# Kernel optimization log

Measured on AMD Instinct MI355X. Metric: run time of the kernel, lower is better.

The kernel has to match this reference:

```python
import jax, jax.numpy as jnp
import numpy as np

LRELU_SLOPE = 0.2
ACT_GAIN = float(np.sqrt(2.0))  # def_gain of lrelu in StyleGAN2
CLAMP = 256.0


def _affine(w, W, b):
    # StyleGAN2 FullyConnectedLayer: runtime weight gain 1/sqrt(in_features)
    return w @ W.T * (1.0 / np.sqrt(W.shape[1])) + b[None, :]


def _gather(x, fn, pad):
    # zero rows for padding faces appended at the end, then neighborhood gather
    padded = jnp.concatenate([x, jnp.zeros((pad, x.shape[1]), x.dtype)], axis=0)
    return padded[fn]  # [N, K, C]


def _mod_texture_conv(g, styles, wc, wsd, wcr):
    # g: [N, 9, I] gathered neighborhoods; styles: [B, I]
    B, I = styles.shape
    N = g.shape[0]
    F = N // B
    # position-typed 1x1 weights: [self, 4 sides, 4 corners] -> [O, I, 9]
    W = jnp.concatenate([wc[:, :, None],
                         jnp.repeat(wsd[:, :, None], 4, axis=2),
                         jnp.repeat(wcr[:, :, None], 4, axis=2)], axis=2)
    wmod = W[None] * styles[:, None, :, None]                    # [B,O,I,9] modulate
    d = jax.lax.rsqrt(jnp.sum(wmod * wmod, axis=(2, 3)) + 1e-8)  # [B,O] demodulate
    wmod = wmod * d[:, :, None, None]
    out = jnp.einsum('bfki,boik->bfok', g.reshape(B, F, 9, I), wmod)
    return out.max(axis=3).reshape(N, -1)  # MaxPool2d((1,9)) aggregation


def _smooth_upsample(x, pool_map, fn, pad):
    # replicate coarse face features to fine faces, then smooth over 9-neighborhood
    return _gather(x[pool_map], fn, pad).mean(axis=1)


def _act(x, bias):
    # clamp_gain(lrelu(x+b), act_gain*gain, 256*gain) with gain=1
    return jnp.clip(jax.nn.leaky_relu(x + bias[None, :], LRELU_SLOPE) * ACT_GAIN, -CLAMP, CLAMP)


def setup_inputs() -> dict:
    key = jax.random.key(0)
    ks = iter(jax.random.split(key, 40))
    B, Fc, Ff = 1, 32768, 131072
    IN, OUT, GEO, COL, WD = 128, 128, 32, 3, 512
    OC1 = OUT - GEO  # 96
    PAD0, PAD1 = 1024, 4096
    nk = lambda *s: jax.random.normal(next(ks), s, jnp.float32)
    ri = lambda shape, hi: jax.random.randint(next(ks), shape, 0, hi, jnp.int32).astype(jnp.int64)
    return dict(
        x=nk(B * Fc, IN - GEO), shape_feat=nk(B * Fc, GEO), img=nk(B * Fc, COL),
        ws=nk(B, 3, WD),
        fn0=ri((B * Fc, 9), B * Fc + PAD0), fn1=ri((B * Ff, 9), B * Ff + PAD1),
        pool_map0=ri((B * Ff,), B * Fc),
        pad0=PAD0, pad1=PAD1,
        affine0_w=nk(IN, WD), affine0_b=jnp.ones((IN,), jnp.float32),
        w_center0=nk(OUT, IN), w_side0=nk(OUT, IN), w_corner0=nk(OUT, IN),
        noise_strength0=nk(1) * 0.1, bias0=nk(OUT) * 0.1, noise_const0=nk(Ff),
        affine1_w=nk(OUT, WD), affine1_b=jnp.ones((OUT,), jnp.float32),
        w_center1=nk(OC1, OUT), w_side1=nk(OC1, OUT), w_corner1=nk(OC1, OUT),
        noise_strength1=nk(1) * 0.1, bias1=nk(OC1) * 0.1, noise_const1=nk(Ff),
        affine2_w=nk(OC1, WD), affine2_b=jnp.ones((OC1,), jnp.float32),
        w_rgb=nk(COL, OC1), bias_rgb=nk(COL) * 0.1,
    )


def reference(x, shape_feat, img, ws, fn0, fn1, pool_map0, pad0, pad1,
              affine0_w, affine0_b, w_center0, w_side0, w_corner0,
              noise_strength0, bias0, noise_const0,
              affine1_w, affine1_b, w_center1, w_side1, w_corner1,
              noise_strength1, bias1, noise_const1,
              affine2_w, affine2_b, w_rgb, bias_rgb):
    B = ws.shape[0]
    h = jnp.concatenate([x, shape_feat], axis=1)  # [B*Fc, IN]
    # ---- conv0: coarse-level modulated face conv, then SmoothUpsample to fine ----
    s0 = _affine(ws[:, 0], affine0_w, affine0_b)
    h = _mod_texture_conv(_gather(h, fn0, pad0), s0, w_center0, w_side0, w_corner0)
    h = _smooth_upsample(h, pool_map0, fn1, pad1)  # [B*Ff, OUT]
    h = h + jnp.tile(noise_const0[None, :], (B, 1)).reshape(-1, 1) * noise_strength0
    h = _act(h, bias0)
    # ---- conv1: fine-level modulated face conv ----
    s1 = _affine(ws[:, 1], affine1_w, affine1_b)
    h = _mod_texture_conv(_gather(h, fn1, pad1), s1, w_center1, w_side1, w_corner1)
    h = h + jnp.tile(noise_const1[None, :], (B, 1)).reshape(-1, 1) * noise_strength1
    h = _act(h, bias1)  # [B*Ff, 96]
    # ---- torgb: 1x1 modulated conv (demodulate=False), weight_gain on styles ----
    s2 = _affine(ws[:, 2], affine2_w, affine2_b) * (1.0 / np.sqrt(w_rgb.shape[1]))
    xg = _gather(h, fn1[:, :1], pad1)[:, 0]  # kernel_size^2 == 1 -> self gather
    y = jnp.einsum('bfi,oi,bi->bfo', xg.reshape(B, -1, xg.shape[1]), w_rgb, s2)
    y = jnp.clip(y.reshape(xg.shape[0], -1) + bias_rgb[None, :], -CLAMP, CLAMP)
    img_out = _smooth_upsample(img, pool_map0, fn1, pad1) + y
    return h, img_out
```

## Files before the change

kernel.cpp:

```cpp
#include <hip/hip_runtime.h>

#define FC 32768
#define FF 131072
#define LRELU_SLOPE 0.2f
#define ACT_GAIN 1.4142135623730951f
#define CLAMP_V 256.0f

typedef __bf16 bf16x8 __attribute__((ext_vector_type(8)));
typedef float f32x4 __attribute__((ext_vector_type(4)));
typedef float f32x2 __attribute__((ext_vector_type(2)));
typedef unsigned u32x4 __attribute__((ext_vector_type(4)));
typedef unsigned u32x2 __attribute__((ext_vector_type(2)));
typedef unsigned short u16x4 __attribute__((ext_vector_type(4)));

static __device__ __forceinline__ unsigned short f2bf(float f) {
    unsigned u = __float_as_uint(f);
    u += 0x7FFFu + ((u >> 16) & 1u);
    return (unsigned short)(u >> 16);
}
static __device__ __forceinline__ unsigned packbf(float a, float b) {
    return (unsigned)f2bf(a) | ((unsigned)f2bf(b) << 16);
}
static __device__ __forceinline__ float bf2f(unsigned short u) {
    return __uint_as_float(((unsigned)u) << 16);
}
static __device__ __forceinline__ float actf(float v) {
    v = (v < 0.f) ? v * LRELU_SLOPE : v;
    v *= ACT_GAIN;
    return fminf(fmaxf(v, -CLAMP_V), CLAMP_V);
}

__global__ void k_prep2(const float* __restrict__ wsvec,
                        const float* __restrict__ a0w, const float* __restrict__ a0b,
                        const float* __restrict__ a1w, const float* __restrict__ a1b,
                        const float* __restrict__ a2w, const float* __restrict__ a2b,
                        float* __restrict__ s0, float* __restrict__ s1, float* __restrict__ s2,
                        unsigned* __restrict__ zrow)
{
    int lane = threadIdx.x & 63;
    int t = blockIdx.x * 4 + (threadIdx.x >> 6);
    if (t >= 352) {
        if (t == 352) zrow[lane] = 0u;
        return;
    }
    int level, o;
    const float *W, *bptr; float* out;
    if (t < 128)       { level = 0; o = t;       W = a0w; bptr = a0b; out = s0; }
    else if (t < 256)  { level = 1; o = t - 128; W = a1w; bptr = a1b; out = s1; }
    else               { level = 2; o = t - 256; W = a2w; bptr = a2b; out = s2; }
    const float* wrow = wsvec + level * 512;
    const float* Wr = W + (size_t)o * 512;
    f32x4 wa = *(const f32x4*)(wrow + lane * 8);
    f32x4 wb = *(const f32x4*)(wrow + lane * 8 + 4);
    f32x4 va = *(const f32x4*)(Wr + lane * 8);
    f32x4 vb = *(const f32x4*)(Wr + lane * 8 + 4);
    float acc = wa.x * va.x + wa.y * va.y + wa.z * va.z + wa.w * va.w
              + wb.x * vb.x + wb.y * vb.y + wb.z * vb.z + wb.w * vb.w;
    #pragma unroll
    for (int off = 32; off; off >>= 1) acc += __shfl_down(acc, off, 64);
    if (lane == 0) {
        float v = acc * 0.04419417382415922f + bptr[o];
        if (level == 2) v *= 0.10206207261596577f;
        out[o] = v;
    }
}

__global__ void k_misc(const float* __restrict__ x, const float* __restrict__ sf,
                       u16x4* __restrict__ xcat,
                       const int* __restrict__ fn1, const int* __restrict__ pmap,
                       int* __restrict__ cidx)
{
    int b = blockIdx.x;
    if (b < FC * 32 / 256) {
        int gid = b * 256 + threadIdx.x;
        int f = gid >> 5;
        int c4 = (gid & 31) * 4;
        f32x4 v;
        if (c4 < 96) v = *(const f32x4*)(x + (size_t)f * 96 + c4);
        else         v = *(const f32x4*)(sf + (size_t)f * 32 + (c4 - 96));
        u16x4 o;
        o.x = f2bf(v.x); o.y = f2bf(v.y); o.z = f2bf(v.z); o.w = f2bf(v.w);
        xcat[gid] = o;
    } else {
        int gid = (b - FC * 32 / 256) * 256 + threadIdx.x;
        int g = fn1[gid];
        cidx[gid] = ((unsigned)g < FF) ? pmap[g] : -1;
    }
}

__global__ void k_wmod(const float* __restrict__ wc0, const float* __restrict__ wsd0,
                       const float* __restrict__ wcr0, const float* __restrict__ s0,
                       unsigned short* __restrict__ wm0,
                       const float* __restrict__ wc1, const float* __restrict__ wsd1,
                       const float* __restrict__ wcr1, const float* __restrict__ s1,
                       unsigned short* __restrict__ wm1,
                       const float* __restrict__ wrgb, const float* __restrict__ s2,
                       float* __restrict__ wrgbmod)
{
    int b = blockIdx.x;
    int i = threadIdx.x;
    if (b == 224) {
        for (int t = i; t < 288; t += 128) {
            int c = t / 96, k = t % 96;
            wrgbmod[c * 96 + k] = wrgb[c * 96 + k] * s2[k];
        }
        return;
    }
    const float *wc, *wsd, *wcr, *s; unsigned short* out; int o, O;
    if (b < 128) { wc = wc0; wsd = wsd0; wcr = wcr0; s = s0; out = wm0; o = b; O = 128; }
    else         { wc = wc1; wsd = wsd1; wcr = wcr1; s = s1; out = wm1; o = b - 128; O = 96; }
    float sv = s[i];
    float pc = wc[o * 128 + i] * sv;
    float ps = wsd[o * 128 + i] * sv;
    float pr = wcr[o * 128 + i] * sv;
    float part = pc * pc + 4.f * ps * ps + 4.f * pr * pr;
    __shared__ float red[2];
    #pragma unroll
    for (int off = 32; off; off >>= 1) part += __shfl_down(part, off, 64);
    if ((threadIdx.x & 63) == 0) red[threadIdx.x >> 6] = part;
    __syncthreads();
    float d = rsqrtf(red[0] + red[1] + 1e-8f);
    out[(0 * O + o) * 128 + i] = f2bf(pc * d);
    out[(1 * O + o) * 128 + i] = f2bf(ps * d);
    out[(2 * O + o) * 128 + i] = f2bf(pr * d);
}

__launch_bounds__(256, 2)
__global__ void k_fgemm0(const unsigned short* __restrict__ xcat,
                         const unsigned short* __restrict__ wm,
                         const int* __restrict__ fn0,
                         const unsigned* __restrict__ zrow,
                         unsigned* __restrict__ hc0)
{
    int lane = threadIdx.x & 63;
    int w = threadIdx.x >> 6;
    int fgrp = w >> 1;
    int mtb = (w & 1) * 4;
    int fbase = (blockIdx.x * 2 + fgrp) * 32;
    int quad = lane >> 4, l15 = lane & 15;
    const char* hb = (const char*)xcat;
    const char* wb = (const char*)wm;

    f32x4 ymax[2][4];
    #pragma unroll
    for (int nt = 0; nt < 2; ++nt)
        #pragma unroll
        for (int mi = 0; mi < 4; ++mi)
            #pragma unroll
            for (int r = 0; r < 4; ++r) ymax[nt][mi][r] = -3.0e38f;

    #pragma unroll
    for (int j = 0; j < 9; ++j) {
        const int t = (j == 0) ? 0 : ((j < 5) ? 1 : 2);
        bf16x8 bfr[2][4];
        #pragma unroll
        for (int nt = 0; nt < 2; ++nt) {
            int idj = fn0[(size_t)(fbase + nt * 16 + l15) * 9 + j];
            const char* src = ((unsigned)idj < FC) ? (hb + (size_t)idj * 256) : (const char*)zrow;
            #pragma unroll
            for (int s = 0; s < 4; ++s)
                bfr[nt][s] = *(const bf16x8*)(src + s * 64 + quad * 16);
        }
        f32x4 acc[2][4];
        #pragma unroll
        for (int nt = 0; nt < 2; ++nt)
            #pragma unroll
            for (int mi = 0; mi < 4; ++mi)
                #pragma unroll
                for (int r = 0; r < 4; ++r) acc[nt][mi][r] = 0.f;
        #pragma unroll
        for (int s = 0; s < 4; ++s) {
            #pragma unroll
            for (int mi = 0; mi < 4; ++mi) {
                bf16x8 afr = *(const bf16x8*)(wb + (size_t)(((t * 128 + (mtb + mi) * 16 + l15) * 128 + s * 32 + quad * 8) * 2));
                acc[0][mi] = __builtin_amdgcn_mfma_f32_16x16x32_bf16(afr, bfr[0][s], acc[0][mi], 0, 0, 0);
                acc[1][mi] = __builtin_amdgcn_mfma_f32_16x16x32_bf16(afr, bfr[1][s], acc[1][mi], 0, 0, 0);
            }
        }
        #pragma unroll
        for (int nt = 0; nt < 2; ++nt)
            #pragma unroll
            for (int mi = 0; mi < 4; ++mi)
                #pragma unroll
                for (int r = 0; r < 4; ++r)
                    ymax[nt][mi][r] = fmaxf(ymax[nt][mi][r], acc[nt][mi][r]);
    }

    #pragma unroll
    for (int nt = 0; nt < 2; ++nt) {
        int face = fbase + nt * 16 + l15;
        #pragma unroll
        for (int mi = 0; mi < 4; ++mi) {
            u32x2 v;
            v.x = packbf(ymax[nt][mi][0], ymax[nt][mi][1]);
            v.y = packbf(ymax[nt][mi][2], ymax[nt][mi][3]);
            *(u32x2*)(hc0 + (size_t)face * 64 + (mtb + mi) * 8 + quad * 2) = v;
        }
    }
}

__global__ void k_upsample(const unsigned* __restrict__ hc, const int* __restrict__ cidx,
                           const float* __restrict__ nco0,
                           const float* __restrict__ ns0p, const float* __restrict__ bias0,
                           unsigned* __restrict__ h1u, const unsigned* __restrict__ zrow)
{
    int gid = blockIdx.x * 256 + threadIdx.x;
    int f = gid >> 4;
    int c = gid & 15;
    int id[9];
    #pragma unroll
    for (int j = 0; j < 9; ++j) id[j] = cidx[f * 9 + j];
    u32x4 v[9];
    #pragma unroll
    for (int j = 0; j < 9; ++j) {
        const unsigned* p = (id[j] >= 0) ? (hc + (size_t)id[j] * 64) : zrow;
        v[j] = *(const u32x4*)(p + c * 4);
    }
    float nz = nco0[f] * ns0p[0];
    f32x4 b0 = *(const f32x4*)(bias0 + c * 8);
    f32x4 b1 = *(const f32x4*)(bias0 + c * 8 + 4);
    const float inv9 = 1.f / 9.f;
    u32x4 out;
    #pragma unroll
    for (int k = 0; k < 4; ++k) {
        float a0 = 0.f, a1 = 0.f;
        #pragma unroll
        for (int j = 0; j < 9; ++j) {
            a0 += bf2f((unsigned short)v[j][k]);
            a1 += bf2f((unsigned short)(v[j][k] >> 16));
        }
        float bb0 = (k < 2) ? ((k == 0) ? b0.x : b0.z) : ((k == 2) ? b1.x : b1.z);
        float bb1 = (k < 2) ? ((k == 0) ? b0.y : b0.w) : ((k == 2) ? b1.y : b1.w);
        a0 = actf(a0 * inv9 + nz + bb0);
        a1 = actf(a1 * inv9 + nz + bb1);
        out[k] = packbf(a0, a1);
    }
    *(u32x4*)(h1u + (size_t)f * 64 + c * 4) = out;
}

__launch_bounds__(256, 2)
__global__ void k_fgemm1(const unsigned short* __restrict__ h1,
                         const unsigned short* __restrict__ wm,
                         const int* __restrict__ fn1,
                         const unsigned* __restrict__ zrow,
                         const float* __restrict__ nco1, const float* __restrict__ ns1p,
                         const float* __restrict__ bias1, const float* __restrict__ wrgbmod,
                         float* __restrict__ hout, f32x4* __restrict__ rgb3)
{
    int lane = threadIdx.x & 63;
    int w = threadIdx.x >> 6;
    int fbase = (blockIdx.x * 4 + w) * 32;
    int quad = lane >> 4, l15 = lane & 15;
    const char* hb = (const char*)h1;
    const char* wb = (const char*)wm;

    f32x4 ymax[2][6];
    #pragma unroll
    for (int nt = 0; nt < 2; ++nt)
        #pragma unroll
        for (int mt = 0; mt < 6; ++mt)
            #pragma unroll
            for (int r = 0; r < 4; ++r) ymax[nt][mt][r] = -3.0e38f;

    #pragma unroll
    for (int j = 0; j < 9; ++j) {
        const int t = (j == 0) ? 0 : ((j < 5) ? 1 : 2);
        bf16x8 bfr[2][4];
        #pragma unroll
        for (int nt = 0; nt < 2; ++nt) {
            int idj = fn1[(size_t)(fbase + nt * 16 + l15) * 9 + j];
            const char* src = ((unsigned)idj < FF) ? (hb + (size_t)idj * 256) : (const char*)zrow;
            #pragma unroll
            for (int s = 0; s < 4; ++s)
                bfr[nt][s] = *(const bf16x8*)(src + s * 64 + quad * 16);
        }
        f32x4 acc[2][6];
        #pragma unroll
        for (int nt = 0; nt < 2; ++nt)
            #pragma unroll
            for (int mt = 0; mt < 6; ++mt)
                #pragma unroll
                for (int r = 0; r < 4; ++r) acc[nt][mt][r] = 0.f;
        #pragma unroll
        for (int s = 0; s < 4; ++s) {
            #pragma unroll
            for (int mt = 0; mt < 6; ++mt) {
                bf16x8 afr = *(const bf16x8*)(wb + (size_t)(((t * 96 + mt * 16 + l15) * 128 + s * 32 + quad * 8) * 2));
                acc[0][mt] = __builtin_amdgcn_mfma_f32_16x16x32_bf16(afr, bfr[0][s], acc[0][mt], 0, 0, 0);
                acc[1][mt] = __builtin_amdgcn_mfma_f32_16x16x32_bf16(afr, bfr[1][s], acc[1][mt], 0, 0, 0);
            }
        }
        #pragma unroll
        for (int nt = 0; nt < 2; ++nt)
            #pragma unroll
            for (int mt = 0; mt < 6; ++mt)
                #pragma unroll
                for (int r = 0; r < 4; ++r)
                    ymax[nt][mt][r] = fmaxf(ymax[nt][mt][r], acc[nt][mt][r]);
    }

    float ns1 = ns1p[0];
    #pragma unroll
    for (int nt = 0; nt < 2; ++nt) {
        int face = fbase + nt * 16 + l15;
        float nz = nco1[face] * ns1;
        float p0 = 0.f, p1 = 0.f, p2 = 0.f;
        #pragma unroll
        for (int mt = 0; mt < 6; ++mt) {
            f32x4 bv = *(const f32x4*)(bias1 + mt * 16 + quad * 4);
            f32x4 hv;
            #pragma unroll
            for (int r = 0; r < 4; ++r) hv[r] = actf(ymax[nt][mt][r] + nz + bv[r]);
            *(f32x4*)(hout + (size_t)face * 96 + mt * 16 + quad * 4) = hv;
            f32x4 w0 = *(const f32x4*)(wrgbmod + mt * 16 + quad * 4);
            f32x4 w1 = *(const f32x4*)(wrgbmod + 96 + mt * 16 + quad * 4);
            f32x4 w2 = *(const f32x4*)(wrgbmod + 192 + mt * 16 + quad * 4);
            p0 += hv.x * w0.x + hv.y * w0.y + hv.z * w0.z + hv.w * w0.w;
            p1 += hv.x * w1.x + hv.y * w1.y + hv.z * w1.z + hv.w * w1.w;
            p2 += hv.x * w2.x + hv.y * w2.y + hv.z * w2.z + hv.w * w2.w;
        }
        p0 += __shfl_xor(p0, 16, 64); p0 += __shfl_xor(p0, 32, 64);
        p1 += __shfl_xor(p1, 16, 64); p1 += __shfl_xor(p1, 32, 64);
        p2 += __shfl_xor(p2, 16, 64); p2 += __shfl_xor(p2, 32, 64);
        if (quad == 0) {
            f32x4 o; o.x = p0; o.y = p1; o.z = p2; o.w = 0.f;
            rgb3[face] = o;
        }
    }
}

__global__ void k_torgb2(const f32x4* __restrict__ rgb3, const int* __restrict__ fn1,
                         const int* __restrict__ cidx, const float* __restrict__ img,
                         const float* __restrict__ brgb, float* __restrict__ imgout)
{
    int f = blockIdx.x * 256 + threadIdx.x;
    int g0 = fn1[(size_t)f * 9];
    float y0 = 0.f, y1 = 0.f, y2 = 0.f;
    if ((unsigned)g0 < FF) {
        f32x4 y = rgb3[g0];
        y0 = y.x; y1 = y.y; y2 = y.z;
    }
    y0 = fminf(fmaxf(y0 + brgb[0], -CLAMP_V), CLAMP_V);
    y1 = fminf(fmaxf(y1 + brgb[1], -CLAMP_V), CLAMP_V);
    y2 = fminf(fmaxf(y2 + brgb[2], -CLAMP_V), CLAMP_V);
    float i0 = 0.f, i1 = 0.f, i2 = 0.f;
    #pragma unroll
    for (int j = 0; j < 9; ++j) {
        int id = cidx[f * 9 + j];
        if (id >= 0) {
            const float* ir = img + (size_t)id * 3;
            i0 += ir[0]; i1 += ir[1]; i2 += ir[2];
        }
    }
    const float inv9 = 1.f / 9.f;
    imgout[(size_t)f * 3 + 0] = i0 * inv9 + y0;
    imgout[(size_t)f * 3 + 1] = i1 * inv9 + y1;
    imgout[(size_t)f * 3 + 2] = i2 * inv9 + y2;
}

extern "C" void kernel_launch(void* const* d_in, const int* in_sizes, int n_in,
                              void* d_out, int out_size, void* d_ws, size_t ws_size,
                              hipStream_t stream) {
    const float* x     = (const float*)d_in[0];
    const float* sfeat = (const float*)d_in[1];
    const float* img   = (const float*)d_in[2];
    const float* wsv   = (const float*)d_in[3];
    const int* fn0     = (const int*)d_in[4];
    const int* fn1     = (const int*)d_in[5];
    const int* pmap    = (const int*)d_in[6];
    const float* a0w   = (const float*)d_in[9];
    const float* a0b   = (const float*)d_in[10];
    const float* wc0   = (const float*)d_in[11];
    const float* wsd0  = (const float*)d_in[12];
    const float* wcr0  = (const float*)d_in[13];
    const float* ns0   = (const float*)d_in[14];
    const float* bias0 = (const float*)d_in[15];
    const float* nco0  = (const float*)d_in[16];
    const float* a1w   = (const float*)d_in[17];
    const float* a1b   = (const float*)d_in[18];
    const float* wc1   = (const float*)d_in[19];
    const float* wsd1  = (const float*)d_in[20];
    const float* wcr1  = (const float*)d_in[21];
    const float* ns1   = (const float*)d_in[22];
    const float* bias1 = (const float*)d_in[23];
    const float* nco1  = (const float*)d_in[24];
    const float* a2w   = (const float*)d_in[25];
    const float* a2b   = (const float*)d_in[26];
    const float* wrgb  = (const float*)d_in[27];
    const float* brgb  = (const float*)d_in[28];

    char* wsb = (char*)d_ws;
    float* s0            = (float*)(wsb + 0);
    float* s1            = (float*)(wsb + 512);
    float* s2            = (float*)(wsb + 1024);
    float* wrgbmod       = (float*)(wsb + 1536);
    unsigned* zrow       = (unsigned*)(wsb + 4096);
    unsigned short* wm0  = (unsigned short*)(wsb + 8192);
    unsigned short* wm1  = (unsigned short*)(wsb + 8192 + 98304);
    unsigned short* xcat = (unsigned short*)(wsb + 262144);
    unsigned* hc0        = (unsigned*)(wsb + 33816576);
    unsigned short* h1   = (unsigned short*)(wsb + 42205184);
    int* cidx            = (int*)(wsb + 75759616);
    f32x4* rgb3          = (f32x4*)(wsb + 155975680);

    float* out_h   = (float*)d_out;
    float* out_img = out_h + (size_t)FF * 96;

    k_misc<<<FC * 32 / 256 + FF * 9 / 256, 256, 0, stream>>>(x, sfeat, (u16x4*)xcat, fn1, pmap, cidx);
    k_prep2<<<89, 256, 0, stream>>>(wsv, a0w, a0b, a1w, a1b, a2w, a2b, s0, s1, s2, zrow);
    k_wmod<<<225, 128, 0, stream>>>(wc0, wsd0, wcr0, s0, wm0,
                                    wc1, wsd1, wcr1, s1, wm1, wrgb, s2, wrgbmod);
    k_fgemm0<<<FC / 64, 256, 0, stream>>>(xcat, wm0, fn0, zrow, hc0);
    k_upsample<<<FF * 16 / 256, 256, 0, stream>>>(hc0, cidx, nco0, ns0, bias0, (unsigned*)h1, zrow);
    k_fgemm1<<<FF / 128, 256, 0, stream>>>(h1, wm1, fn1, zrow, nco1, ns1, bias1, wrgbmod,
                                           out_h, rgb3);
    k_torgb2<<<FF / 256, 256, 0, stream>>>(rgb3, fn1, cidx, img, brgb, out_img);
}
```

Measured before the change: 326.6 us.

## Shrink per-wave face tiles in face GEMMs to raise occupancy, add nontemporal stores

Both face-conv GEMM kernels now give each wave 16 faces instead of 32, covering all output channels per wave. The 9 neighbor indices are loaded up front and launch bounds go from 2 to 4 blocks per SM. This cuts accumulator registers so more waves can hide gather latency, at the cost of reloading weight fragments for every 16 faces instead of 32. Intermediate and output stores switch to nontemporal hints to reduce cache pollution, which risks evicting data that the next kernel rereads.

New measurement: 604.2 us. +85.0%, slower.

```diff
diff --git a/kernel.cpp b/kernel.cpp
--- a/kernel.cpp
+++ b/kernel.cpp
@@ -80,7 +80,7 @@
         else         v = *(const f32x4*)(sf + (size_t)f * 32 + (c4 - 96));
         u16x4 o;
         o.x = f2bf(v.x); o.y = f2bf(v.y); o.z = f2bf(v.z); o.w = f2bf(v.w);
-        xcat[gid] = o;
+        __builtin_nontemporal_store(o, &xcat[gid]);
     } else {
         int gid = (b - FC * 32 / 256) * 256 + threadIdx.x;
         int g = fn1[gid];
@@ -125,7 +125,7 @@
     out[(2 * O + o) * 128 + i] = f2bf(pr * d);
 }
 
-__launch_bounds__(256, 2)
+__launch_bounds__(256, 4)
 __global__ void k_fgemm0(const unsigned short* __restrict__ xcat,
                          const unsigned short* __restrict__ wm,
                          const int* __restrict__ fn0,
@@ -134,68 +134,56 @@
 {
     int lane = threadIdx.x & 63;
     int w = threadIdx.x >> 6;
-    int fgrp = w >> 1;
-    int mtb = (w & 1) * 4;
-    int fbase = (blockIdx.x * 2 + fgrp) * 32;
+    int fbase = (blockIdx.x * 4 + w) * 16;
     int quad = lane >> 4, l15 = lane & 15;
+    int face = fbase + l15;
     const char* hb = (const char*)xcat;
     const char* wb = (const char*)wm;
 
-    f32x4 ymax[2][4];
-    #pragma unroll
-    for (int nt = 0; nt < 2; ++nt)
-        #pragma unroll
-        for (int mi = 0; mi < 4; ++mi)
-            #pragma unroll
-            for (int r = 0; r < 4; ++r) ymax[nt][mi][r] = -3.0e38f;
+    int id[9];
+    #pragma unroll
+    for (int j = 0; j < 9; ++j) id[j] = fn0[(size_t)face * 9 + j];
+
+    f32x4 ymax[8];
+    #pragma unroll
+    for (int mt = 0; mt < 8; ++mt)
+        #pragma unroll
+        for (int r = 0; r < 4; ++r) ymax[mt][r] = -3.0e38f;
 
     #pragma unroll
     for (int j = 0; j < 9; ++j) {
         const int t = (j == 0) ? 0 : ((j < 5) ? 1 : 2);
-        bf16x8 bfr[2][4];
-        #pragma unroll
-        for (int nt = 0; nt < 2; ++nt) {
-            int idj = fn0[(size_t)(fbase + nt * 16 + l15) * 9 + j];
-            const char* src = ((unsigned)idj < FC) ? (hb + (size_t)idj * 256) : (const char*)zrow;
-            #pragma unroll
-            for (int s = 0; s < 4; ++s)
-                bfr[nt][s] = *(const bf16x8*)(src + s * 64 + quad * 16);
-        }
-        f32x4 acc[2][4];
-        #pragma unroll
-        for (int nt = 0; nt < 2; ++nt)
-            #pragma unroll
-            for (int mi = 0; mi < 4; ++mi)
-                #pragma unroll
-                for (int r = 0; r < 4; ++r) acc[nt][mi][r] = 0.f;
+        const char* src = ((unsigned)id[j] < FC) ? (hb + (size_t)id[j] * 256) : (const char*)zrow;
+        bf16x8 bfr[4];
+        #pragma unroll
+        for (int s = 0; s < 4; ++s)
+            bfr[s] = *(const bf16x8*)(src + s * 64 + quad * 16);
+        f32x4 acc[8];
+        #pragma unroll
+        for (int mt = 0; mt < 8; ++mt)
+            #pragma unroll
+            for (int r = 0; r < 4; ++r) acc[mt][r] = 0.f;
         #pragma unroll
         for (int s = 0; s < 4; ++s) {
             #pragma unroll
-            for (int mi = 0; mi < 4; ++mi) {
-                bf16x8 afr = *(const bf16x8*)(wb + (size_t)(((t * 128 + (mtb + mi) * 16 + l15) * 128 + s * 32 + quad * 8) * 2));
-                acc[0][mi] = __builtin_amdgcn_mfma_f32_16x16x32_bf16(afr, bfr[0][s], acc[0][mi], 0, 0, 0);
-                acc[1][mi] = __builtin_amdgcn_mfma_f32_16x16x32_bf16(afr, bfr[1][s], acc[1][mi], 0, 0, 0);
+            for (int mt = 0; mt < 8; ++mt) {
+                bf16x8 afr = *(const bf16x8*)(wb + (size_t)(((t * 128 + mt * 16 + l15) * 128 + s * 32 + quad * 8) * 2));
+                acc[mt] = __builtin_amdgcn_mfma_f32_16x16x32_bf16(afr, bfr[s], acc[mt], 0, 0, 0);
             }
         }
         #pragma unroll
-        for (int nt = 0; nt < 2; ++nt)
-            #pragma unroll
-            for (int mi = 0; mi < 4; ++mi)
-                #pragma unroll
-                for (int r = 0; r < 4; ++r)
-                    ymax[nt][mi][r] = fmaxf(ymax[nt][mi][r], acc[nt][mi][r]);
-    }
-
-    #pragma unroll
-    for (int nt = 0; nt < 2; ++nt) {
-        int face = fbase + nt * 16 + l15;
-        #pragma unroll
-        for (int mi = 0; mi < 4; ++mi) {
-            u32x2 v;
-            v.x = packbf(ymax[nt][mi][0], ymax[nt][mi][1]);
-            v.y = packbf(ymax[nt][mi][2], ymax[nt][mi][3]);
-            *(u32x2*)(hc0 + (size_t)face * 64 + (mtb + mi) * 8 + quad * 2) = v;
-        }
+        for (int mt = 0; mt < 8; ++mt)
+            #pragma unroll
+            for (int r = 0; r < 4; ++r)
+                ymax[mt][r] = fmaxf(ymax[mt][r], acc[mt][r]);
+    }
+
+    #pragma unroll
+    for (int mt = 0; mt < 8; ++mt) {
+        u32x2 v;
+        v.x = packbf(ymax[mt][0], ymax[mt][1]);
+        v.y = packbf(ymax[mt][2], ymax[mt][3]);
+        __builtin_nontemporal_store(v, (u32x2*)(hc0 + (size_t)face * 64 + mt * 8 + quad * 2));
     }
 }
 
@@ -235,10 +223,10 @@
         a1 = actf(a1 * inv9 + nz + bb1);
         out[k] = packbf(a0, a1);
     }
-    *(u32x4*)(h1u + (size_t)f * 64 + c * 4) = out;
-}
-
-__launch_bounds__(256, 2)
+    __builtin_nontemporal_store(out, (u32x4*)(h1u + (size_t)f * 64 + c * 4));
+}
+
+__launch_bounds__(256, 4)
 __global__ void k_fgemm1(const unsigned short* __restrict__ h1,
                          const unsigned short* __restrict__ wm,
                          const int* __restrict__ fn1,
@@ -249,83 +237,73 @@
 {
     int lane = threadIdx.x & 63;
     int w = threadIdx.x >> 6;
-    int fbase = (blockIdx.x * 4 + w) * 32;
+    int fbase = (blockIdx.x * 4 + w) * 16;
     int quad = lane >> 4, l15 = lane & 15;
+    int face = fbase + l15;
     const char* hb = (const char*)h1;
     const char* wb = (const char*)wm;
 
-    f32x4 ymax[2][6];
-    #pragma unroll
-    for (int nt = 0; nt < 2; ++nt)
-        #pragma unroll
-        for (int mt = 0; mt < 6; ++mt)
-            #pragma unroll
-            for (int r = 0; r < 4; ++r) ymax[nt][mt][r] = -3.0e38f;
+    int id[9];
+    #pragma unroll
+    for (int j = 0; j < 9; ++j) id[j] = fn1[(size_t)face * 9 + j];
+
+    f32x4 ymax[6];
+    #pragma unroll
+    for (int mt = 0; mt < 6; ++mt)
+        #pragma unroll
+        for (int r = 0; r < 4; ++r) ymax[mt][r] = -3.0e38f;
 
     #pragma unroll
     for (int j = 0; j < 9; ++j) {
         const int t = (j == 0) ? 0 : ((j < 5) ? 1 : 2);
-        bf16x8 bfr[2][4];
-        #pragma unroll
-        for (int nt = 0; nt < 2; ++nt) {
-            int idj = fn1[(size_t)(fbase + nt * 16 + l15) * 9 + j];
-            const char* src = ((unsigned)idj < FF) ? (hb + (size_t)idj * 256) : (const char*)zrow;
-            #pragma unroll
-            for (int s = 0; s < 4; ++s)
-                bfr[nt][s] = *(const bf16x8*)(src + s * 64 + quad * 16);
-        }
-        f32x4 acc[2][6];
-        #pragma unroll
-        for (int nt = 0; nt < 2; ++nt)
-            #pragma unroll
-            for (int mt = 0; mt < 6; ++mt)
-                #pragma unroll
-                for (int r = 0; r < 4; ++r) acc[nt][mt][r] = 0.f;
+        const char* src = ((unsigned)id[j] < FF) ? (hb + (size_t)id[j] * 256) : (const char*)zrow;
+        bf16x8 bfr[4];
+        #pragma unroll
+        for (int s = 0; s < 4; ++s)
+            bfr[s] = *(const bf16x8*)(src + s * 64 + quad * 16);
+        f32x4 acc[6];
+        #pragma unroll
+        for (int mt = 0; mt < 6; ++mt)
+            #pragma unroll
+            for (int r = 0; r < 4; ++r) acc[mt][r] = 0.f;
         #pragma unroll
         for (int s = 0; s < 4; ++s) {
             #pragma unroll
             for (int mt = 0; mt < 6; ++mt) {
                 bf16x8 afr = *(const bf16x8*)(wb + (size_t)(((t * 96 + mt * 16 + l15) * 128 + s * 32 + quad * 8) * 2));
-                acc[0][mt] = __builtin_amdgcn_mfma_f32_16x16x32_bf16(afr, bfr[0][s], acc[0][mt], 0, 0, 0);
-                acc[1][mt] = __builtin_amdgcn_mfma_f32_16x16x32_bf16(afr, bfr[1][s], acc[1][mt], 0, 0, 0);
+                acc[mt] = __builtin_amdgcn_mfma_f32_16x16x32_bf16(afr, bfr[s], acc[mt], 0, 0, 0);
             }
         }
         #pragma unroll
-        for (int nt = 0; nt < 2; ++nt)
-            #pragma unroll
-            for (int mt = 0; mt < 6; ++mt)
-                #pragma unroll
-                for (int r = 0; r < 4; ++r)
-                    ymax[nt][mt][r] = fmaxf(ymax[nt][mt][r], acc[nt][mt][r]);
+        for (int mt = 0; mt < 6; ++mt)
+            #pragma unroll
+            for (int r = 0; r < 4; ++r)
+                ymax[mt][r] = fmaxf(ymax[mt][r], acc[mt][r]);
     }
 
     float ns1 = ns1p[0];
-    #pragma unroll
-    for (int nt = 0; nt < 2; ++nt) {
-        int face = fbase + nt * 16 + l15;
-        float nz = nco1[face] * ns1;
-        float p0 = 0.f, p1 = 0.f, p2 = 0.f;
-        #pragma unroll
-        for (int mt = 0; mt < 6; ++mt) {
-            f32x4 bv = *(const f32x4*)(bias1 + mt * 16 + quad * 4);
-            f32x4 hv;
-            #pragma unroll
-            for (int r = 0; r < 4; ++r) hv[r] = actf(ymax[nt][mt][r] + nz + bv[r]);
-            *(f32x4*)(hout + (size_t)face * 96 + mt * 16 + quad * 4) = hv;
-            f32x4 w0 = *(const f32x4*)(wrgbmod + mt * 16 + quad * 4);
-            f32x4 w1 = *(const f32x4*)(wrgbmod + 96 + mt * 16 + quad * 4);
-            f32x4 w2 = *(const f32x4*)(wrgbmod + 192 + mt * 16 + quad * 4);
-            p0 += hv.x * w0.x + hv.y * w0.y + hv.z * w0.z + hv.w * w0.w;
-            p1 += hv.x * w1.x + hv.y * w1.y + hv.z * w1.z + hv.w * w1.w;
-            p2 += hv.x * w2.x + hv.y * w2.y + hv.z * w2.z + hv.w * w2.w;
-        }
-        p0 += __shfl_xor(p0, 16, 64); p0 += __shfl_xor(p0, 32, 64);
-        p1 += __shfl_xor(p1, 16, 64); p1 += __shfl_xor(p1, 32, 64);
-        p2 += __shfl_xor(p2, 16, 64); p2 += __shfl_xor(p2, 32, 64);
-        if (quad == 0) {
-            f32x4 o; o.x = p0; o.y = p1; o.z = p2; o.w = 0.f;
-            rgb3[face] = o;
-        }
+    float nz = nco1[face] * ns1;
+    float p0 = 0.f, p1 = 0.f, p2 = 0.f;
+    #pragma unroll
+    for (int mt = 0; mt < 6; ++mt) {
+        f32x4 bv = *(const f32x4*)(bias1 + mt * 16 + quad * 4);
+        f32x4 hv;
+        #pragma unroll
+        for (int r = 0; r < 4; ++r) hv[r] = actf(ymax[mt][r] + nz + bv[r]);
+        __builtin_nontemporal_store(hv, (f32x4*)(hout + (size_t)face * 96 + mt * 16 + quad * 4));
+        f32x4 w0 = *(const f32x4*)(wrgbmod + mt * 16 + quad * 4);
+        f32x4 w1 = *(const f32x4*)(wrgbmod + 96 + mt * 16 + quad * 4);
+        f32x4 w2 = *(const f32x4*)(wrgbmod + 192 + mt * 16 + quad * 4);
+        p0 += hv.x * w0.x + hv.y * w0.y + hv.z * w0.z + hv.w * w0.w;
+        p1 += hv.x * w1.x + hv.y * w1.y + hv.z * w1.z + hv.w * w1.w;
+        p2 += hv.x * w2.x + hv.y * w2.y + hv.z * w2.z + hv.w * w2.w;
+    }
+    p0 += __shfl_xor(p0, 16, 64); p0 += __shfl_xor(p0, 32, 64);
+    p1 += __shfl_xor(p1, 16, 64); p1 += __shfl_xor(p1, 32, 64);
+    p2 += __shfl_xor(p2, 16, 64); p2 += __shfl_xor(p2, 32, 64);
+    if (quad == 0) {
+        f32x4 o; o.x = p0; o.y = p1; o.z = p2; o.w = 0.f;
+        __builtin_nontemporal_store(o, &rgb3[face]);
     }
 }
 
@@ -412,7 +390,7 @@
                                     wc1, wsd1, wcr1, s1, wm1, wrgb, s2, wrgbmod);
     k_fgemm0<<<FC / 64, 256, 0, stream>>>(xcat, wm0, fn0, zrow, hc0);
     k_upsample<<<FF * 16 / 256, 256, 0, stream>>>(hc0, cidx, nco0, ns0, bias0, (unsigned*)h1, zrow);
-    k_fgemm1<<<FF / 128, 256, 0, stream>>>(h1, wm1, fn1, zrow, nco1, ns1, bias1, wrgbmod,
-                                           out_h, rgb3);
+    k_fgemm1<<<FF / 64, 256, 0, stream>>>(h1, wm1, fn1, zrow, nco1, ns1, bias1, wrgbmod,
+                                          out_h, rgb3);
     k_torgb2<<<FF / 256, 256, 0, stream>>>(rgb3, fn1, cidx, img, brgb, out_img);
 }
```
